# Optimization experiments

Measured on AMD Instinct MI355X. Metric: run time of the kernel, lower is better.

The kernel has to match this reference:

```python
import jax, jax.numpy as jnp
import numpy as np

EPS_NORM = 1e-12
BN_EPS = 1e-5

def _l2norm(x, axis=-1):
    n = jnp.sqrt(jnp.sum(x * x, axis=axis, keepdims=True))
    return x / jnp.maximum(n, EPS_NORM)

def setup_inputs() -> dict:
    key = jax.random.key(0)
    ks = jax.random.split(key, 16)
    B, C, H, W, K = 32, 256, 64, 64, 5
    supp_feat = jax.random.normal(ks[0], (B, C, H, W), dtype=jnp.float32)
    supp_mask = (jax.random.uniform(ks[1], (B, 1, H, W)) > 0.5).astype(jnp.float32)
    part_queries = 0.02 * jax.random.normal(ks[2], (1, K, C), dtype=jnp.float32)
    temperature = jnp.array([0.1], dtype=jnp.float32)
    margin = jnp.array([0.15], dtype=jnp.float32)
    q_w = jax.random.normal(ks[3], (C, C), dtype=jnp.float32) / np.sqrt(C)  # 1x1 conv, no bias
    bn_w = 1.0 + 0.1 * jax.random.normal(ks[4], (C,), dtype=jnp.float32)
    bn_b = 0.1 * jax.random.normal(ks[5], (C,), dtype=jnp.float32)
    bn_mean = 0.1 * jax.random.normal(ks[6], (C,), dtype=jnp.float32)
    bn_var = 0.5 + jax.random.uniform(ks[7], (C,), dtype=jnp.float32)
    k_w = jax.random.normal(ks[8], (C, C), dtype=jnp.float32) / np.sqrt(C)
    k_b = 0.01 * jax.random.normal(ks[9], (C,), dtype=jnp.float32)
    v_w = jax.random.normal(ks[10], (C, C), dtype=jnp.float32) / np.sqrt(C)
    v_b = 0.01 * jax.random.normal(ks[11], (C,), dtype=jnp.float32)
    out_w = jax.random.normal(ks[12], (C, C), dtype=jnp.float32) / np.sqrt(C)
    out_b = 0.01 * jax.random.normal(ks[13], (C,), dtype=jnp.float32)
    gamma = jnp.array([0.1], dtype=jnp.float32)  # nonzero so the refine branch contributes
    return {"supp_feat": supp_feat, "supp_mask": supp_mask, "part_queries": part_queries,
            "temperature": temperature, "margin": margin, "q_w": q_w, "bn_w": bn_w,
            "bn_b": bn_b, "bn_mean": bn_mean, "bn_var": bn_var, "k_w": k_w, "k_b": k_b,
            "v_w": v_w, "v_b": v_b, "out_w": out_w, "out_b": out_b, "gamma": gamma}

def reference(supp_feat, supp_mask, part_queries, temperature, margin, q_w, bn_w, bn_b,
              bn_mean, bn_var, k_w, k_b, v_w, v_b, out_w, out_b, gamma):
    B, C, H, W = supp_feat.shape
    K = part_queries.shape[1]
    flat_mask = supp_mask.reshape(B, -1)                       # [B, HW]
    flat_feat = jnp.swapaxes(supp_feat.reshape(B, C, -1), 1, 2)  # [B, HW, C]
    queries_norm = _l2norm(part_queries)[0]                    # [K, C]
    feat_norm = _l2norm(flat_feat)                             # [B, HW, C]
    temp = jnp.maximum(temperature, 0.01)[0]
    sim = jnp.einsum('kc,bnc->bkn', queries_norm, feat_norm) / temp  # [B, K, HW]
    sim = jnp.where(flat_mask[:, None, :] > 0, sim, -jnp.inf)
    attn = jnp.nan_to_num(jax.nn.softmax(sim, axis=-1), nan=0.0)
    part_tokens = jnp.einsum('bkn,bnc->bkc', attn, flat_feat)  # [B, K, C]
    # diversity loss
    nt = _l2norm(part_tokens)
    cos = jnp.einsum('bkc,bjc->bkj', nt, nt) * (1.0 - jnp.eye(K, dtype=supp_feat.dtype))
    m = jnp.clip(margin, 0.0, 0.5)[0]
    div_loss = jnp.maximum(cos - m, 0.0).sum() / (B * K * (K - 1) + 1e-5)
    # refine attention
    q = jnp.einsum('oc,bchw->bohw', q_w, supp_feat)            # 1x1 conv, no bias
    scale = bn_w / jnp.sqrt(bn_var + BN_EPS)
    q = q * scale[None, :, None, None] + (bn_b - bn_mean * scale)[None, :, None, None]
    Q = jnp.swapaxes(q.reshape(B, C, -1), 1, 2)                # [B, HW, C]
    Kt = part_tokens @ k_w.T + k_b                             # [B, K, C]
    Vt = part_tokens @ v_w.T + v_b
    refine = jax.nn.softmax(jnp.einsum('bnc,bkc->bnk', Q, Kt) / (C ** 0.5), axis=-1)
    attn_out = jnp.einsum('bnk,bkc->bnc', refine, Vt)          # [B, HW, C]
    attn_out = jnp.swapaxes(attn_out, 1, 2).reshape(B, C, H, W)
    attn_out = jnp.einsum('oc,bchw->bohw', out_w, attn_out) + out_b[None, :, None, None]
    enhanced = supp_feat + gamma[0] * attn_out
    return (enhanced, div_loss, part_tokens)
```

## Files before the change

kernel.cpp:

```cpp
#include <hip/hip_runtime.h>
#include <hip/hip_bf16.h>
#include <math.h>

#define B_  32
#define C_  256
#define HW_ 4096
#define K_  5
#define P_  128
#define NT_ 32

typedef __hip_bfloat16 bf16;
typedef unsigned int u32;

template<bool BF>
__device__ inline float LD(const void* p, size_t i) {
    if (BF) return __bfloat162float(((const bf16*)p)[i]);
    return ((const float*)p)[i];
}
template<bool BF>
__device__ inline void ST(void* p, size_t i, float v) {
    if (BF) ((bf16*)p)[i] = __float2bfloat16(v);
    else    ((float*)p)[i] = v;
}
template<bool BF>
__device__ inline float4 LD4(const void* p, size_t i) {
    if (BF) {
        ushort4 u = *(const ushort4*)((const unsigned short*)p + i);
        float4 r;
        r.x = __uint_as_float(((u32)u.x) << 16);
        r.y = __uint_as_float(((u32)u.y) << 16);
        r.z = __uint_as_float(((u32)u.z) << 16);
        r.w = __uint_as_float(((u32)u.w) << 16);
        return r;
    }
    return *(const float4*)((const float*)p + i);
}
template<bool BF>
__device__ inline void ST2(void* p, size_t i, float2 v) {
    if (BF) {
        bf16 a = __float2bfloat16(v.x), b = __float2bfloat16(v.y);
        ushort2 u;
        u.x = *(unsigned short*)&a; u.y = *(unsigned short*)&b;
        *(ushort2*)((unsigned short*)p + i) = u;
    } else {
        *(float2*)((float*)p + i) = v;
    }
}
__device__ inline u32 packbf2(float a, float b) {
    bf16 x = __float2bfloat16(a), y = __float2bfloat16(b);
    return (((u32)*(unsigned short*)&y) << 16) | (u32)(*(unsigned short*)&x);
}
__device__ inline float lo16f(u32 u) { return __uint_as_float(u << 16); }
__device__ inline float hi16f(u32 u) { return __uint_as_float(u & 0xffff0000u); }

__device__ int detect_bf(const void* feat, int* cntL) {
    int t = threadIdx.x;
    if (t == 0) *cntL = 0;
    __syncthreads();
    const unsigned short* u = (const unsigned short*)feat;
    int local = 0;
    for (int i = t; i < 4096; i += blockDim.x) {
        float v = __uint_as_float(((u32)u[i]) << 16);
        float a = fabsf(v);
        if (a >= 1e-4f && a <= 100.f) local++;
    }
    atomicAdd(cntL, local);
    __syncthreads();
    return (*cntL > 3072) ? 1 : 0;
}

__device__ inline float blk_sum(float v, float* sh) {
    for (int o = 32; o > 0; o >>= 1) v += __shfl_down(v, o, 64);
    int w = threadIdx.x >> 6;
    __syncthreads();
    if ((threadIdx.x & 63) == 0) sh[w] = v;
    __syncthreads();
    return sh[0] + sh[1] + sh[2] + sh[3];
}

template<bool BF>
__device__ void simpt_body(const void* feat, const void* mask, const void* temp,
                           const void* pq, float* ptp, float* mz, float* smem) {
    u32*   featU = (u32*)smem;
    float* reg   = smem + 16384;
    float* qL    = smem + 16384 + 1920;
    float* simL  = qL;
    float* mL    = qL + 1280;
    float* sc    = mL + 128;
    int t = threadIdx.x, lane = t & 63, q = t >> 6;
    int b = blockIdx.y, tile = blockIdx.x;

    if (q < K_) {
        float4 v = LD4<BF>(pq, (size_t)q * C_ + lane * 4);
        float ss = v.x * v.x + v.y * v.y + v.z * v.z + v.w * v.w;
        for (int o = 32; o > 0; o >>= 1) ss += __shfl_xor(ss, o, 64);
        float inv = 1.0f / fmaxf(sqrtf(ss), 1e-12f);
        *(float4*)(qL + q * C_ + lane * 4) =
            make_float4(v.x * inv, v.y * inv, v.z * inv, v.w * inv);
    }
    if (t == 0) sc[0] = 1.0f / fmaxf(LD<BF>(temp, 0), 0.01f);
    if (t < 32) *(float4*)(mL + t * 4) = LD4<BF>(mask, (size_t)b * HW_ + tile * P_ + t * 4);
    __syncthreads();

    int c0 = q * 32, half = lane >> 5, lm = lane & 31;
    float sa[4] = {0.f, 0.f, 0.f, 0.f};
    float da[K_][4];
    #pragma unroll
    for (int k = 0; k < K_; k++)
        #pragma unroll
        for (int i = 0; i < 4; i++) da[k][i] = 0.f;
    size_t gbase = (size_t)b * C_ * HW_ + (size_t)tile * P_ + lm * 4;
    #pragma unroll 4
    for (int j = 0; j < 16; j++) {
        int c = c0 + 2 * j + half;
        float4 f = LD4<BF>(feat, gbase + (size_t)c * HW_);
        sa[0] += f.x * f.x; sa[1] += f.y * f.y; sa[2] += f.z * f.z; sa[3] += f.w * f.w;
        #pragma unroll
        for (int k = 0; k < K_; k++) {
            float qv = qL[k * C_ + c];
            da[k][0] += f.x * qv; da[k][1] += f.y * qv;
            da[k][2] += f.z * qv; da[k][3] += f.w * qv;
        }
        int ps = lm ^ (c & 31);
        *(uint2*)&featU[c * 64 + 2 * ps] =
            make_uint2(packbf2(f.x, f.y), packbf2(f.z, f.w));
    }
    #pragma unroll
    for (int i = 0; i < 4; i++) sa[i] += __shfl_down(sa[i], 32, 64);
    #pragma unroll
    for (int k = 0; k < K_; k++)
        #pragma unroll
        for (int i = 0; i < 4; i++) da[k][i] += __shfl_down(da[k][i], 32, 64);

    float* red = reg;
    for (int r = 0; r < 4; r++) {
        if (lane < 32) {
            red[0 * 256 + q * 32 + lane] = sa[r];
            #pragma unroll
            for (int k = 0; k < K_; k++) red[(1 + k) * 256 + q * 32 + lane] = da[k][r];
        }
        __syncthreads();
        if (t < 160) {
            int kk = t >> 5, m = t & 31, n = 4 * m + r;
            float ssum = 0.f, dsum = 0.f;
            #pragma unroll
            for (int g = 0; g < 8; g++) {
                ssum += red[0 * 256 + g * 32 + m];
                dsum += red[(1 + kk) * 256 + g * 32 + m];
            }
            simL[kk * P_ + n] = (mL[n] > 0.f)
                ? dsum * (sc[0] / fmaxf(sqrtf(ssum), 1e-12f)) : -INFINITY;
        }
        __syncthreads();
    }

    float* wL   = reg;
    float* psum = reg + 640;
    if (q < K_) {
        float s0 = simL[q * P_ + 2 * lane], s1 = simL[q * P_ + 2 * lane + 1];
        float m = fmaxf(s0, s1);
        for (int o = 32; o > 0; o >>= 1) m = fmaxf(m, __shfl_xor(m, o, 64));
        float e0 = (s0 == -INFINITY) ? 0.f : __expf(s0 - m);
        float e1 = (s1 == -INFINITY) ? 0.f : __expf(s1 - m);
        float z = e0 + e1;
        for (int o = 32; o > 0; o >>= 1) z += __shfl_xor(z, o, 64);
        *(float2*)(wL + q * P_ + 2 * lane) = make_float2(e0, e1);
        if (lane == 0) {
            size_t mzb = ((size_t)(b * NT_ + tile) * K_ + q) * 2;
            mz[mzb] = m; mz[mzb + 1] = z;
        }
    }
    __syncthreads();

    int cch = t & 255, h = t >> 8, x = cch & 31;
    float acc[K_] = {0.f, 0.f, 0.f, 0.f, 0.f};
    #pragma unroll 4
    for (int jj = 0; jj < 16; jj++) {
        int p = h * 16 + jj;
        uint2 v = *(const uint2*)&featU[cch * 64 + 2 * (p ^ x)];
        float f0 = lo16f(v.x), f1 = hi16f(v.x), f2 = lo16f(v.y), f3 = hi16f(v.y);
        #pragma unroll
        for (int k = 0; k < K_; k++) {
            float4 w4 = *(const float4*)(wL + k * P_ + 4 * p);
            acc[k] += f0 * w4.x + f1 * w4.y + f2 * w4.z + f3 * w4.w;
        }
    }
    if (h == 1) {
        #pragma unroll
        for (int k = 0; k < K_; k++) psum[k * C_ + cch] = acc[k];
    }
    __syncthreads();
    if (h == 0) {
        size_t pb = (size_t)(b * NT_ + tile) * (K_ * C_);
        #pragma unroll
        for (int k = 0; k < K_; k++)
            ptp[pb + k * C_ + cch] = acc[k] + psum[k * C_ + cch];
    }
}
__global__ __launch_bounds__(512, 4) void k_simpt(const void* feat, const void* mask,
                                                  const void* temp, const void* pq,
                                                  float* ptp, float* mz) {
    __shared__ __attribute__((aligned(16))) float smem[19720];
    __shared__ int cnt;
    int flg = detect_bf(feat, &cnt);
    if (flg) simpt_body<true >(feat, mask, temp, pq, ptp, mz, smem);
    else     simpt_body<false>(feat, mask, temp, pq, ptp, mz, smem);
}

__device__ inline float merge_one(const float* ptp, const float* mz,
                                  int b, int kk, int c) {
    float M = -INFINITY;
    #pragma unroll 8
    for (int tl = 0; tl < NT_; tl++)
        M = fmaxf(M, mz[((size_t)(b * NT_ + tl) * K_ + kk) * 2]);
    float Zs = 0.f, acc = 0.f;
    #pragma unroll 8
    for (int tl = 0; tl < NT_; tl++) {
        size_t mzb = ((size_t)(b * NT_ + tl) * K_ + kk) * 2;
        float m_t = mz[mzb], z_t = mz[mzb + 1];
        float s = (m_t == -INFINITY) ? 0.f : __expf(m_t - M);
        Zs += z_t * s;
        acc += ptp[(size_t)(b * NT_ + tl) * (K_ * C_) + kk * C_ + c] * s;
    }
    return (Zs > 0.f) ? acc / Zs : 0.f;
}
template<bool BF>
__device__ void prep_part(const void* qw, const void* kw, const void* kb,
                          const void* vw, const void* vb, const void* ow,
                          const void* bnw, const void* bnb, const void* bnm,
                          const void* bnv, float ptv, int bk,
                          float* W2, float* b2, float* OV, float* pt, float* smem) {
    float* ptL = smem;
    float* KtL = smem + 256;
    float* VtL = smem + 512;
    float* sh  = smem + 768;
    int t = threadIdx.x;
    ptL[t] = ptv;
    pt[(size_t)bk * C_ + t] = ptv;
    __syncthreads();
    float kt = LD<BF>(kb, t), vt = LD<BF>(vb, t);
    for (int c = 0; c < C_; c += 4) {
        float4 p4 = *(float4*)(ptL + c);
        float4 kw4 = LD4<BF>(kw, (size_t)t * C_ + c);
        float4 vw4 = LD4<BF>(vw, (size_t)t * C_ + c);
        kt += kw4.x * p4.x + kw4.y * p4.y + kw4.z * p4.z + kw4.w * p4.w;
        vt += vw4.x * p4.x + vw4.y * p4.y + vw4.z * p4.z + vw4.w * p4.w;
    }
    float scale = LD<BF>(bnw, t) * rsqrtf(LD<BF>(bnv, t) + 1e-5f);
    float shift = LD<BF>(bnb, t) - LD<BF>(bnm, t) * scale;
    KtL[t] = kt * scale;
    VtL[t] = vt;
    float bpart = kt * shift;
    __syncthreads();
    float ov = 0;
    for (int c = 0; c < C_; c += 4) {
        float4 v4 = *(float4*)(VtL + c);
        float4 ow4 = LD4<BF>(ow, (size_t)t * C_ + c);
        ov += ow4.x * v4.x + ow4.y * v4.y + ow4.z * v4.z + ow4.w * v4.w;
    }
    OV[(size_t)bk * C_ + t] = ov;
    float w2 = 0;
    for (int o = 0; o < C_; o++) w2 += KtL[o] * LD<BF>(qw, (size_t)o * C_ + t);
    W2[(size_t)bk * C_ + t] = w2 * (1.0f / 16.0f);
    float bs = blk_sum(bpart, sh);
    if (t == 0) b2[bk] = bs * (1.0f / 16.0f);
}
template<bool BF>
__device__ void div_part(const float* ptp, const float* mz, const void* margin,
                         float* divpart, float* smem) {
    float* ptL = smem;
    float* rn  = smem + K_ * C_;
    float* sh  = rn + 8;
    int b = blockIdx.x - B_ * K_, t = threadIdx.x;
    for (int kk = 0; kk < K_; kk++) ptL[kk * C_ + t] = merge_one(ptp, mz, b, kk, t);
    __syncthreads();
    for (int k = 0; k < K_; k++) {
        float v = ptL[k * C_ + t];
        float s = blk_sum(v * v, sh);
        if (t == 0) rn[k] = 1.0f / fmaxf(sqrtf(s), 1e-12f);
    }
    __syncthreads();
    float m = LD<BF>(margin, 0);
    m = fminf(fmaxf(m, 0.f), 0.5f);
    int p = t >> 3, g = t & 7;
    float contrib = 0.f;
    if (p < K_ * K_) {
        int k = p / K_, j = p % K_;
        float d = 0;
        for (int c = g; c < C_; c += 8) d += ptL[k * C_ + c] * ptL[j * C_ + c];
        d += __shfl_down(d, 4, 8);
        d += __shfl_down(d, 2, 8);
        d += __shfl_down(d, 1, 8);
        if (g == 0 && k != j) contrib = fmaxf(d * rn[k] * rn[j] - m, 0.f);
    }
    float s = blk_sum(contrib, sh);
    if (t == 0) divpart[b] = s;
}
template<bool BF>
__device__ void mergeprep_body(const void* qw, const void* kw, const void* kb,
                               const void* vw, const void* vb, const void* ow,
                               const void* bnw, const void* bnb, const void* bnm,
                               const void* bnv, const void* margin,
                               const float* ptp, const float* mz,
                               float* W2, float* b2, float* OV, float* pt,
                               float* divpart, float* smem) {
    int bid = blockIdx.x, t = threadIdx.x;
    if (bid < B_ * K_) {
        int b = bid / K_, kk = bid % K_;
        float ptv = merge_one(ptp, mz, b, kk, t);
        prep_part<BF>(qw, kw, kb, vw, vb, ow, bnw, bnb, bnm, bnv,
                      ptv, bid, W2, b2, OV, pt, smem);
    } else {
        div_part<BF>(ptp, mz, margin, divpart, smem);
    }
}
__global__ void k_mergeprep(const void* feat, const void* qw, const void* kw,
                            const void* kb, const void* vw, const void* vb,
                            const void* ow, const void* bnw, const void* bnb,
                            const void* bnm, const void* bnv, const void* margin,
                            const float* ptp, const float* mz,
                            float* W2, float* b2, float* OV, float* pt, float* divpart) {
    __shared__ __attribute__((aligned(16))) float smem[K_ * C_ + 16];
    __shared__ int cnt;
    int flg = detect_bf(feat, &cnt);
    if (flg) mergeprep_body<true >(qw, kw, kb, vw, vb, ow, bnw, bnb, bnm, bnv, margin,
                                   ptp, mz, W2, b2, OV, pt, divpart, smem);
    else     mergeprep_body<false>(qw, kw, kb, vw, vb, ow, bnw, bnb, bnm, bnv, margin,
                                   ptp, mz, W2, b2, OV, pt, divpart, smem);
}

template<bool BF>
__device__ void fin_body(const void* feat, const void* outb, const void* gamma,
                         const float* W2, const float* b2, const float* OV,
                         const float* pt, const float* divpart,
                         void* dout, float* smem) {
    u32*   featU = (u32*)smem;
    float* red   = smem + 16384;
    float* eL    = red + 1280;
    u32*   W2p   = (u32*)(eL + 640);
    u32*   OVp   = W2p + 640;
    float* obL   = (float*)(OVp + 640);
    float* b2L   = obL + 256;
    int t = threadIdx.x, lane = t & 63, q = t >> 6;
    int b = blockIdx.y, tile = blockIdx.x;
    for (int i = t; i < 640; i += 512) {
        W2p[i] = packbf2(W2[(size_t)b * 1280 + 2 * i], W2[(size_t)b * 1280 + 2 * i + 1]);
        OVp[i] = packbf2(OV[(size_t)b * 1280 + 2 * i], OV[(size_t)b * 1280 + 2 * i + 1]);
    }
    if (t < C_) obL[t] = LD<BF>(outb, t);
    if (t < K_) b2L[t] = b2[b * K_ + t];
    __syncthreads();

    int c0 = q * 32, half = lane >> 5, lm = lane & 31;
    size_t gbase = (size_t)b * C_ * HW_ + (size_t)tile * P_ + lm * 4;
    float la[K_][4];
    #pragma unroll
    for (int k = 0; k < K_; k++)
        #pragma unroll
        for (int i = 0; i < 4; i++) la[k][i] = 0.f;
    #pragma unroll 4
    for (int j = 0; j < 16; j++) {
        int c = c0 + 2 * j + half;
        float4 f = LD4<BF>(feat, gbase + (size_t)c * HW_);
        #pragma unroll
        for (int k = 0; k < K_; k++) {
            u32 u = W2p[k * 128 + (c >> 1)];
            float wv = half ? hi16f(u) : lo16f(u);
            la[k][0] += f.x * wv; la[k][1] += f.y * wv;
            la[k][2] += f.z * wv; la[k][3] += f.w * wv;
        }
        int ps = lm ^ (c & 31);
        *(uint2*)&featU[c * 64 + 2 * ps] =
            make_uint2(packbf2(f.x, f.y), packbf2(f.z, f.w));
    }
    #pragma unroll
    for (int k = 0; k < K_; k++)
        #pragma unroll
        for (int i = 0; i < 4; i++) la[k][i] += __shfl_down(la[k][i], 32, 64);

    for (int r = 0; r < 4; r++) {
        if (lane < 32) {
            #pragma unroll
            for (int k = 0; k < K_; k++) red[k * 256 + q * 32 + lane] = la[k][r];
        }
        __syncthreads();
        if (t < 32) {
            int n = 4 * t + r;
            float lg[K_];
            #pragma unroll
            for (int k = 0; k < K_; k++) {
                float s = b2L[k];
                #pragma unroll
                for (int g = 0; g < 8; g++) s += red[k * 256 + g * 32 + t];
                lg[k] = s;
            }
            float mx = fmaxf(fmaxf(fmaxf(lg[0], lg[1]), fmaxf(lg[2], lg[3])), lg[4]);
            float e0 = __expf(lg[0] - mx), e1 = __expf(lg[1] - mx),
                  e2 = __expf(lg[2] - mx), e3 = __expf(lg[3] - mx),
                  e4 = __expf(lg[4] - mx);
            float inv = 1.0f / (e0 + e1 + e2 + e3 + e4);
            eL[0 * P_ + n] = e0 * inv; eL[1 * P_ + n] = e1 * inv;
            eL[2 * P_ + n] = e2 * inv; eL[3 * P_ + n] = e3 * inv;
            eL[4 * P_ + n] = e4 * inv;
        }
        __syncthreads();
    }

    float g = LD<BF>(gamma, 0);
    float2 ek[K_];
    #pragma unroll
    for (int k = 0; k < K_; k++) ek[k] = *(const float2*)(eL + k * P_ + 2 * lane);
    size_t obase = (size_t)b * C_ * HW_ + (size_t)tile * P_ + 2 * lane;
    #pragma unroll 4
    for (int cc = 0; cc < 32; cc++) {
        int c = c0 + cc, x = c & 31;
        u32 v = featU[c * 64 + 2 * ((lane >> 1) ^ x) + (lane & 1)];
        float f0 = lo16f(v), f1 = hi16f(v);
        float ob = obL[c];
        float a0 = ob, a1 = ob;
        #pragma unroll
        for (int k = 0; k < K_; k++) {
            u32 u = OVp[k * 128 + (c >> 1)];
            float ov = (c & 1) ? hi16f(u) : lo16f(u);
            a0 += ek[k].x * ov; a1 += ek[k].y * ov;
        }
        ST2<BF>(dout, obase + (size_t)c * HW_, make_float2(f0 + g * a0, f1 + g * a1));
    }
    if (b == 0) {
        const size_t enh = (size_t)B_ * C_ * HW_;
        for (int i = blockIdx.x * 512 + t; i < B_ * K_ * C_; i += NT_ * 512)
            ST<BF>(dout, enh + 1 + i, pt[i]);
        if (blockIdx.x == 0 && t == 0) {
            float s = 0;
            for (int bb = 0; bb < B_; bb++) s += divpart[bb];
            ST<BF>(dout, enh, s / (640.0f + 1e-5f));
        }
    }
}
__global__ __launch_bounds__(512, 4) void k_fin(const void* feat, const void* outb,
                                                const void* gamma, const float* W2,
                                                const float* b2, const float* OV,
                                                const float* pt, const float* divpart,
                                                void* dout) {
    __shared__ __attribute__((aligned(16))) float smem[19848];
    __shared__ int cnt;
    int flg = detect_bf(feat, &cnt);
    if (flg) fin_body<true >(feat, outb, gamma, W2, b2, OV, pt, divpart, dout, smem);
    else     fin_body<false>(feat, outb, gamma, W2, b2, OV, pt, divpart, dout, smem);
}

extern "C" void kernel_launch(void* const* d_in, const int* in_sizes, int n_in,
                              void* d_out, int out_size, void* d_ws, size_t ws_size,
                              hipStream_t stream) {
    const void* feat = d_in[0];
    const void* mask = d_in[1];
    const void* pq   = d_in[2];
    const void* temp = d_in[3];
    const void* marg = d_in[4];
    const void* qw   = d_in[5];
    const void* bnw  = d_in[6];
    const void* bnb  = d_in[7];
    const void* bnm  = d_in[8];
    const void* bnv  = d_in[9];
    const void* kw   = d_in[10];
    const void* kb   = d_in[11];
    const void* vw   = d_in[12];
    const void* vb   = d_in[13];
    const void* ow   = d_in[14];
    const void* ob   = d_in[15];
    const void* gm   = d_in[16];

    float* ws  = (float*)d_ws;
    float* ptp = ws;
    float* mz  = ptp + (size_t)B_ * NT_ * K_ * C_;
    float* pt  = mz  + (size_t)B_ * NT_ * K_ * 2;
    float* W2  = pt  + B_ * K_ * C_;
    float* b2  = W2  + B_ * K_ * C_;
    float* OV  = b2  + B_ * K_;
    float* dvp = OV  + B_ * K_ * C_;

    hipLaunchKernelGGL(k_simpt, dim3(NT_, B_), dim3(512), 0, stream,
                       feat, mask, temp, pq, ptp, mz);
    hipLaunchKernelGGL(k_mergeprep, dim3(B_ * K_ + B_), dim3(256), 0, stream,
                       feat, qw, kw, kb, vw, vb, ow, bnw, bnb, bnm, bnv, marg,
                       ptp, mz, W2, b2, OV, pt, dvp);
    hipLaunchKernelGGL(k_fin, dim3(NT_, B_), dim3(512), 0, stream,
                       feat, ob, gm, W2, b2, OV, pt, dvp, d_out);
}
```

Before: 161.7 us.

## Compute part-token weighted sums with bf16 MFMA instead of scalar FMAs

Result: faster. 148.5 us (-8.2%).

```diff
diff --git a/kernel.cpp b/kernel.cpp
--- a/kernel.cpp
+++ b/kernel.cpp
@@ -8,9 +8,12 @@
 #define K_  5
 #define P_  128
 #define NT_ 32
+#define PS_ 68
 
 typedef __hip_bfloat16 bf16;
 typedef unsigned int u32;
+typedef __attribute__((ext_vector_type(8))) short bf16x8;
+typedef __attribute__((ext_vector_type(4))) float f32x4;
 
 template<bool BF>
 __device__ inline float LD(const void* p, size_t i) {
@@ -62,9 +65,10 @@
     for (int i = t; i < 4096; i += blockDim.x) {
         float v = __uint_as_float(((u32)u[i]) << 16);
         float a = fabsf(v);
-        if (a >= 1e-4f && a <= 100.f) local++;
-    }
-    atomicAdd(cntL, local);
+        local += (a >= 1e-4f && a <= 100.f) ? 1 : 0;
+    }
+    for (int o = 32; o > 0; o >>= 1) local += __shfl_down(local, o, 64);
+    if ((t & 63) == 0) atomicAdd(cntL, local);
     __syncthreads();
     return (*cntL > 3072) ? 1 : 0;
 }
@@ -81,12 +85,12 @@
 template<bool BF>
 __device__ void simpt_body(const void* feat, const void* mask, const void* temp,
                            const void* pq, float* ptp, float* mz, float* smem) {
-    u32*   featU = (u32*)smem;
-    float* reg   = smem + 16384;
-    float* qL    = smem + 16384 + 1920;
+    u32*   featB = (u32*)smem;
+    float* red   = smem + 17408;
+    u32*   wB    = (u32*)red;
+    float* qL    = smem + 17408 + 1536;
     float* simL  = qL;
-    float* mL    = qL + 1280;
-    float* sc    = mL + 128;
+    float* sc    = qL + 1280;
     int t = threadIdx.x, lane = t & 63, q = t >> 6;
     int b = blockIdx.y, tile = blockIdx.x;
 
@@ -99,7 +103,6 @@
             make_float4(v.x * inv, v.y * inv, v.z * inv, v.w * inv);
     }
     if (t == 0) sc[0] = 1.0f / fmaxf(LD<BF>(temp, 0), 0.01f);
-    if (t < 32) *(float4*)(mL + t * 4) = LD4<BF>(mask, (size_t)b * HW_ + tile * P_ + t * 4);
     __syncthreads();
 
     int c0 = q * 32, half = lane >> 5, lm = lane & 31;
@@ -121,8 +124,7 @@
             da[k][0] += f.x * qv; da[k][1] += f.y * qv;
             da[k][2] += f.z * qv; da[k][3] += f.w * qv;
         }
-        int ps = lm ^ (c & 31);
-        *(uint2*)&featU[c * 64 + 2 * ps] =
+        *(uint2*)&featB[c * PS_ + 2 * lm] =
             make_uint2(packbf2(f.x, f.y), packbf2(f.z, f.w));
     }
     #pragma unroll
@@ -132,7 +134,7 @@
         #pragma unroll
         for (int i = 0; i < 4; i++) da[k][i] += __shfl_down(da[k][i], 32, 64);
 
-    float* red = reg;
+    float tinv = sc[0];
     for (int r = 0; r < 4; r++) {
         if (lane < 32) {
             red[0 * 256 + q * 32 + lane] = sa[r];
@@ -148,14 +150,13 @@
                 ssum += red[0 * 256 + g * 32 + m];
                 dsum += red[(1 + kk) * 256 + g * 32 + m];
             }
-            simL[kk * P_ + n] = (mL[n] > 0.f)
-                ? dsum * (sc[0] / fmaxf(sqrtf(ssum), 1e-12f)) : -INFINITY;
+            float mval = LD<BF>(mask, (size_t)b * HW_ + tile * P_ + n);
+            simL[kk * P_ + n] = (mval > 0.f)
+                ? dsum * (tinv / fmaxf(sqrtf(ssum), 1e-12f)) : -INFINITY;
         }
         __syncthreads();
     }
 
-    float* wL   = reg;
-    float* psum = reg + 640;
     if (q < K_) {
         float s0 = simL[q * P_ + 2 * lane], s1 = simL[q * P_ + 2 * lane + 1];
         float m = fmaxf(s0, s1);
@@ -164,7 +165,7 @@
         float e1 = (s1 == -INFINITY) ? 0.f : __expf(s1 - m);
         float z = e0 + e1;
         for (int o = 32; o > 0; o >>= 1) z += __shfl_xor(z, o, 64);
-        *(float2*)(wL + q * P_ + 2 * lane) = make_float2(e0, e1);
+        wB[q * PS_ + lane] = packbf2(e0, e1);
         if (lane == 0) {
             size_t mzb = ((size_t)(b * NT_ + tile) * K_ + q) * 2;
             mz[mzb] = m; mz[mzb + 1] = z;
@@ -172,35 +173,29 @@
     }
     __syncthreads();
 
-    int cch = t & 255, h = t >> 8, x = cch & 31;
-    float acc[K_] = {0.f, 0.f, 0.f, 0.f, 0.f};
-    #pragma unroll 4
-    for (int jj = 0; jj < 16; jj++) {
-        int p = h * 16 + jj;
-        uint2 v = *(const uint2*)&featU[cch * 64 + 2 * (p ^ x)];
-        float f0 = lo16f(v.x), f1 = hi16f(v.x), f2 = lo16f(v.y), f3 = hi16f(v.y);
-        #pragma unroll
-        for (int k = 0; k < K_; k++) {
-            float4 w4 = *(const float4*)(wL + k * P_ + 4 * p);
-            acc[k] += f0 * w4.x + f1 * w4.y + f2 * w4.z + f3 * w4.w;
-        }
-    }
-    if (h == 1) {
-        #pragma unroll
-        for (int k = 0; k < K_; k++) psum[k * C_ + cch] = acc[k];
-    }
-    __syncthreads();
-    if (h == 0) {
-        size_t pb = (size_t)(b * NT_ + tile) * (K_ * C_);
-        #pragma unroll
-        for (int k = 0; k < K_; k++)
-            ptp[pb + k * C_ + cch] = acc[k] + psum[k * C_ + cch];
+    int r16 = lane & 15, g = lane >> 4;
+    size_t pb = (size_t)(b * NT_ + tile) * (K_ * C_);
+    #pragma unroll
+    for (int sub = 0; sub < 2; sub++) {
+        int ctile = q * 32 + sub * 16;
+        f32x4 acc = {0.f, 0.f, 0.f, 0.f};
+        #pragma unroll
+        for (int s = 0; s < 4; s++) {
+            bf16x8 a = *(const bf16x8*)(featB + (ctile + r16) * PS_ + 16 * s + 4 * g);
+            bf16x8 bb = *(const bf16x8*)(wB + r16 * PS_ + 16 * s + 4 * g);
+            acc = __builtin_amdgcn_mfma_f32_16x16x32_bf16(a, bb, acc, 0, 0, 0);
+        }
+        if (r16 < K_) {
+            #pragma unroll
+            for (int r = 0; r < 4; r++)
+                ptp[pb + (size_t)r16 * C_ + ctile + 4 * g + r] = acc[r];
+        }
     }
 }
 __global__ __launch_bounds__(512, 4) void k_simpt(const void* feat, const void* mask,
                                                   const void* temp, const void* pq,
                                                   float* ptp, float* mz) {
-    __shared__ __attribute__((aligned(16))) float smem[19720];
+    __shared__ __attribute__((aligned(16))) float smem[20232];
     __shared__ int cnt;
     int flg = detect_bf(feat, &cnt);
     if (flg) simpt_body<true >(feat, mask, temp, pq, ptp, mz, smem);
```
